# Kernel tuning notes

Hardware: AMD Instinct MI355X
Metric: run time of the kernel (lower is better)

The kernel has to match this reference:

```python
import jax, jax.numpy as jnp
import numpy as np

HEADS = 8
DIM_HEAD = 64
NH = 16
NW = 16
SCALE = DIM_HEAD ** -0.5


def _avg2x2(a):
    # 2x2 average pool, stride 1, over axes 1,2 of [B,H,W,C] (== unfold+mean in torch)
    return (a[:, :-1, :-1] + a[:, 1:, :-1] + a[:, :-1, 1:] + a[:, 1:, 1:]) * 0.25


def _split_heads(t):
    B, n, _ = t.shape
    return t.reshape(B, n, HEADS, DIM_HEAD).transpose(0, 2, 1, 3)  # b h n d


def setup_inputs() -> dict:
    key = jax.random.key(0)
    ks = jax.random.split(key, 5)
    B, n, dim = 64, 482, 512
    inner = HEADS * DIM_HEAD
    return {
        "x": jax.random.normal(ks[0], (B, n, dim), jnp.float32),
        "mask": jax.random.normal(ks[1], (B, n, dim), jnp.float32),
        "W_qkv": jax.random.normal(ks[2], (3 * inner, dim), jnp.float32) * 0.02,
        "W_out": jax.random.normal(ks[3], (dim, inner), jnp.float32) * 0.02,
        "b_out": jax.random.normal(ks[4], (dim,), jnp.float32) * 0.02,
    }


def reference(x, mask, W_qkv, W_out, b_out):
    sg = jax.lax.stop_gradient
    B, n, dim = x.shape
    inner = HEADS * DIM_HEAD
    nHW = NH * NW            # 256
    nb = (NH - 1) * (NW - 1)  # 225

    # qkv projection
    qkv = x @ W_qkv.T                              # [B,n,3*inner]
    q, k, v = (
        _split_heads(t) for t in jnp.split(qkv, 3, axis=-1)
    )

    # mask path (no grad)
    mask_ = sg(mask)
    updated = (jnp.mean(mask_[:, 1:], axis=-1, keepdims=True) > 0.0).astype(x.dtype)
    updated = jnp.concatenate([jnp.ones_like(updated[:, :1]), updated], axis=1)  # [B,n,1]
    qkv_m = mask_ @ jnp.abs(sg(W_qkv)).T
    q_m, k_m, v_m = (_split_heads(t) for t in jnp.split(qkv_m, 3, axis=-1))
    q_m = q_m / (1e-6 + jnp.max(q_m, axis=2, keepdims=True))
    k_m = k_m / (1e-6 + jnp.max(k_m, axis=2, keepdims=True))
    v_m = v_m / (1e-6 + jnp.max(v_m, axis=2, keepdims=True))
    q_m, k_m, v_m = sg(q_m), sg(k_m), sg(v_m)

    # mask-modulated attention
    dots = jnp.einsum('bhnd,bhmd->bhnm', q * q_m, k * k_m) * SCALE
    attn = jax.nn.softmax(dots, axis=-1)
    out = jnp.einsum('bhnm,bhmd->bhnd', attn, v_m * v)
    out = out.transpose(0, 2, 1, 3).reshape(B, n, inner) * updated

    m = jnp.einsum('bhnm,bhmd->bhnd', sg(attn), v_m)
    m = sg(m.transpose(0, 2, 1, 3).reshape(B, n, inner) * updated)

    # overlap blending (is_overlap=True)
    inv_tail = 1.0 - updated[:, -nb:]
    inv_grid = 1.0 - updated[:, 1:nHW + 1]

    out_bridge = _avg2x2(out[:, 1:nHW + 1].reshape(B, NH, NW, inner)).reshape(B, nb, inner) * inv_tail
    out_origin = jnp.pad(out[:, -nb:].reshape(B, NH - 1, NW - 1, inner),
                         ((0, 0), (1, 1), (1, 1), (0, 0)))
    out_origin = _avg2x2(out_origin).reshape(B, nHW, inner) * inv_grid

    m_bridge = _avg2x2(m[:, 1:nHW + 1].reshape(B, NH, NW, inner)).reshape(B, nb, inner) * inv_tail
    m_origin = jnp.pad(m[:, -nb:].reshape(B, NH - 1, NW - 1, inner),
                       ((0, 0), (1, 1), (1, 1), (0, 0)))
    m_origin = _avg2x2(m_origin).reshape(B, nHW, inner) * inv_grid

    out = out.at[:, 1:nHW + 1].add(out_origin).at[:, -nb:].add(out_bridge)
    m = sg(m.at[:, 1:nHW + 1].add(m_origin).at[:, -nb:].add(m_bridge))

    # nearest-neighbor interpolation of mask means (no grad)
    mm = jnp.mean(m[:, 1:], axis=-1, keepdims=True)          # [B,n-1,1]
    a = mm[:, :nHW].reshape(B, 1, NH, NW)
    inter = jnp.repeat(jnp.repeat(a, 16, axis=2), 16, axis=3)  # [B,1,256,256]
    b = mm[:, -nb:].reshape(B, 1, NH - 1, NW - 1)
    inter_shift = jnp.repeat(jnp.repeat(b, 16, axis=2), 16, axis=3)  # [B,1,240,240]
    inter = inter.at[:, :, 8:-8, 8:-8].set((inter[:, :, 8:-8, 8:-8] + inter_shift) * 0.5)
    inter = sg(inter)

    m = sg(m @ jnp.abs(sg(W_out)).T)

    out_final = out @ W_out.T + b_out
    return out_final, m, inter
```

## Files before the change

### kernel.cpp

```cpp
#include <hip/hip_runtime.h>

#define B_      64
#define NSEQ    482
#define DIM     512
#define HEADS_  8
#define HD      64
#define QKV3    1536
#define NPAD    512
#define MROWS   (B_ * NSEQ)

typedef __bf16 v8bf __attribute__((ext_vector_type(8)));
typedef float  v4f  __attribute__((ext_vector_type(4)));

typedef __attribute__((address_space(1))) const unsigned short gu16;
typedef __attribute__((address_space(3))) unsigned short lu16;

__device__ __forceinline__ unsigned short f2bf(float f) {
    unsigned u = __float_as_uint(f);
    u += 0x7fffu + ((u >> 16) & 1u);
    return (unsigned short)(u >> 16);
}
__device__ __forceinline__ float bf2f(unsigned short h) {
    return __uint_as_float(((unsigned)h) << 16);
}

__global__ void k_cvt(const float* __restrict__ s, unsigned short* __restrict__ d, int n4) {
    int i = blockIdx.x * 256 + threadIdx.x;
    if (i < n4) {
        float4 v = ((const float4*)s)[i];
        ushort4 o;
        o.x = f2bf(v.x); o.y = f2bf(v.y); o.z = f2bf(v.z); o.w = f2bf(v.w);
        ((ushort4*)d)[i] = o;
    }
}

__global__ void k_cvtabs(const float* __restrict__ s, unsigned short* __restrict__ d,
                         unsigned short* __restrict__ da, int n4) {
    int i = blockIdx.x * 256 + threadIdx.x;
    if (i < n4) {
        float4 v = ((const float4*)s)[i];
        ushort4 o, oa;
        o.x = f2bf(v.x); o.y = f2bf(v.y); o.z = f2bf(v.z); o.w = f2bf(v.w);
        oa.x = f2bf(fabsf(v.x)); oa.y = f2bf(fabsf(v.y));
        oa.z = f2bf(fabsf(v.z)); oa.w = f2bf(fabsf(v.w));
        ((ushort4*)d)[i] = o;
        ((ushort4*)da)[i] = oa;
    }
}

__global__ __launch_bounds__(256) void k_cvtmask(const float* __restrict__ mask,
                                                 unsigned short* __restrict__ mb,
                                                 float* __restrict__ upd) {
    int row = blockIdx.x * 4 + (threadIdx.x >> 6);
    int lane = threadIdx.x & 63;
    const float4* p = (const float4*)(mask + (size_t)row * DIM);
    ushort4* d = (ushort4*)(mb + (size_t)row * DIM);
    float s = 0.f;
    #pragma unroll
    for (int j = 0; j < 2; j++) {
        float4 v = p[j * 64 + lane];
        ushort4 o;
        o.x = f2bf(v.x); o.y = f2bf(v.y); o.z = f2bf(v.z); o.w = f2bf(v.w);
        d[j * 64 + lane] = o;
        s += v.x + v.y + v.z + v.w;
    }
    #pragma unroll
    for (int off = 32; off; off >>= 1) s += __shfl_xor(s, off);
    if (lane == 0) {
        int i = row % NSEQ;
        upd[row] = (i == 0) ? 1.f : ((s > 0.f) ? 1.f : 0.f);
    }
}

__global__ __launch_bounds__(256, 2) void k_gemm(const unsigned short* __restrict__ A,
                                                 const unsigned short* __restrict__ Bw,
                                                 unsigned short* __restrict__ Cb,
                                                 float* __restrict__ Cf,
                                                 const float* __restrict__ bias,
                                                 int N, int K) {
    __shared__ __align__(16) unsigned short As[128 * 32];
    __shared__ __align__(16) unsigned short Bs[128 * 32];
    int tid = threadIdx.x;
    int lane = tid & 63, w = tid >> 6;
    int wm = w & 1, wn = w >> 1;
    int quad = lane >> 4, m16 = lane & 15;
    int m0 = blockIdx.y * 128, n0 = blockIdx.x * 128;

    int srow = w * 16 + (lane >> 2);
    int scol = (lane & 3) * 8;
    const unsigned short* gA0 = &A[(size_t)(m0 + srow) * K + scol];
    const unsigned short* gA1 = &A[(size_t)(m0 + 64 + srow) * K + scol];
    const unsigned short* gB0 = &Bw[(size_t)(n0 + srow) * K + scol];
    const unsigned short* gB1 = &Bw[(size_t)(n0 + 64 + srow) * K + scol];
    lu16* lA0 = (lu16*)&As[w * 512];
    lu16* lA1 = (lu16*)&As[2048 + w * 512];
    lu16* lB0 = (lu16*)&Bs[w * 512];
    lu16* lB1 = (lu16*)&Bs[2048 + w * 512];

    v4f acc[4][4];
    #pragma unroll
    for (int i = 0; i < 4; i++)
        #pragma unroll
        for (int j = 0; j < 4; j++) acc[i][j] = (v4f){0.f, 0.f, 0.f, 0.f};

    for (int k0 = 0; k0 < K; k0 += 32) {
        __builtin_amdgcn_global_load_lds((gu16*)(gA0 + k0), lA0, 16, 0, 0);
        __builtin_amdgcn_global_load_lds((gu16*)(gA1 + k0), lA1, 16, 0, 0);
        __builtin_amdgcn_global_load_lds((gu16*)(gB0 + k0), lB0, 16, 0, 0);
        __builtin_amdgcn_global_load_lds((gu16*)(gB1 + k0), lB1, 16, 0, 0);
        __syncthreads();
        v8bf af[4], bf[4];
        #pragma unroll
        for (int i = 0; i < 4; i++)
            af[i] = *(const v8bf*)&As[(wm * 64 + i * 16 + m16) * 32 + quad * 8];
        #pragma unroll
        for (int j = 0; j < 4; j++)
            bf[j] = *(const v8bf*)&Bs[(wn * 64 + j * 16 + m16) * 32 + quad * 8];
        #pragma unroll
        for (int i = 0; i < 4; i++)
            #pragma unroll
            for (int j = 0; j < 4; j++)
                acc[i][j] = __builtin_amdgcn_mfma_f32_16x16x32_bf16(af[i], bf[j], acc[i][j], 0, 0, 0);
        __syncthreads();
    }

    #pragma unroll
    for (int j = 0; j < 4; j++) {
        int col = n0 + wn * 64 + j * 16 + m16;
        float bi = bias ? bias[col] : 0.f;
        #pragma unroll
        for (int i = 0; i < 4; i++) {
            int rowb = m0 + wm * 64 + i * 16 + quad * 4;
            #pragma unroll
            for (int r = 0; r < 4; r++) {
                float v = acc[i][j][r] + bi;
                size_t off = (size_t)(rowb + r) * N + col;
                if (Cf) Cf[off] = v;
                else    Cb[off] = f2bf(v);
            }
        }
    }
}

__global__ void k_colmax(const unsigned short* __restrict__ qm, float* __restrict__ invsc) {
    int b = blockIdx.x;
    int c = blockIdx.y * 256 + threadIdx.x;
    const unsigned short* p = qm + (size_t)b * NSEQ * QKV3 + c;
    float mx = -1e30f;
    for (int i = 0; i < NSEQ; i++) mx = fmaxf(mx, bf2f(p[(size_t)i * QKV3]));
    invsc[b * QKV3 + c] = 1.f / (1e-6f + mx);
}

__global__ __launch_bounds__(256) void k_build(const unsigned short* __restrict__ qkv,
                                               const unsigned short* __restrict__ qm,
                                               const float* __restrict__ invsc,
                                               unsigned short* __restrict__ QQ,
                                               unsigned short* __restrict__ KK,
                                               unsigned short* __restrict__ VVt,
                                               unsigned short* __restrict__ VMt) {
    __shared__ unsigned short tv[64][72];
    __shared__ unsigned short tm[64][72];
    int tid = threadIdx.x;
    int dd = tid & 63, il = tid >> 6;
    int it = blockIdx.x, h = blockIdx.y, b = blockIdx.z;
    int i0 = it * 64;
    size_t bh = (size_t)(b * HEADS_ + h);
    int c = h * HD + dd;
    float invq = invsc[b * QKV3 + c] * 0.125f;
    float invk = invsc[b * QKV3 + 512 + c];
    float invv = invsc[b * QKV3 + 1024 + c];
    #pragma unroll 4
    for (int p = 0; p < 16; p++) {
        int li = p * 4 + il;
        int i = i0 + li;
        unsigned short oq = 0, ok = 0, ov = 0, om = 0;
        if (i < NSEQ) {
            size_t base = ((size_t)(b * NSEQ + i)) * QKV3 + c;
            float q  = bf2f(qkv[base]),        qv = bf2f(qm[base]);
            float kk = bf2f(qkv[base + 512]),  kv = bf2f(qm[base + 512]);
            float vv = bf2f(qkv[base + 1024]), vm = bf2f(qm[base + 1024]);
            oq = f2bf(q * qv * invq);
            ok = f2bf(kk * kv * invk);
            float vmn = vm * invv;
            ov = f2bf(vv * vmn);
            om = f2bf(vmn);
        }
        QQ[(bh * NPAD + i) * HD + dd] = oq;
        KK[(bh * NPAD + i) * HD + dd] = ok;
        tv[li][dd] = ov;
        tm[li][dd] = om;
    }
    __syncthreads();
    #pragma unroll 4
    for (int p = 0; p < 16; p++) {
        int dr = p * 4 + il;
        VVt[(bh * HD + dr) * NPAD + i0 + dd] = tv[dd][dr];
        VMt[(bh * HD + dr) * NPAD + i0 + dd] = tm[dd][dr];
    }
}

__global__ __launch_bounds__(256, 3) void k_attn(const unsigned short* __restrict__ QQ,
                                                 const unsigned short* __restrict__ KK,
                                                 const unsigned short* __restrict__ VVt,
                                                 const unsigned short* __restrict__ VMt,
                                                 const float* __restrict__ upd,
                                                 float* __restrict__ OUT1,
                                                 float* __restrict__ M1) {
    __shared__ __align__(16) unsigned short Ks[2][32 * 72];
    __shared__ __align__(16) unsigned short Vs[2][64 * 40];
    __shared__ __align__(16) unsigned short Ms[2][64 * 40];
    __shared__ __align__(16) unsigned short Ps[4][32 * 40];

    int tid = threadIdx.x;
    int w = tid >> 6, lane = tid & 63;
    int quad = lane >> 4, m16 = lane & 15;
    int b = blockIdx.z, h = blockIdx.y;
    int q0 = blockIdx.x * 128 + w * 32;
    size_t bh = (size_t)(b * HEADS_ + h);

    v8bf aq[2][2];
    #pragma unroll
    for (int s = 0; s < 2; s++) {
        const unsigned short* qb = &QQ[(bh * NPAD + q0 + s * 16 + m16) * HD];
        aq[s][0] = *(const v8bf*)&qb[quad * 8];
        aq[s][1] = *(const v8bf*)&qb[32 + quad * 8];
    }

    v4f vacc[2][4], macc[2][4];
    #pragma unroll
    for (int s = 0; s < 2; s++)
        #pragma unroll
        for (int dt = 0; dt < 4; dt++) {
            vacc[s][dt] = (v4f){0.f, 0.f, 0.f, 0.f};
            macc[s][dt] = (v4f){0.f, 0.f, 0.f, 0.f};
        }
    float lrun[2][4];
    #pragma unroll
    for (int s = 0; s < 2; s++)
        #pragma unroll
        for (int r = 0; r < 4; r++) lrun[s][r] = 0.f;

    const unsigned short* gK = &KK[bh * NPAD * HD + tid * 8];
    const unsigned short* gV = &VVt[(bh * HD + (tid >> 2)) * NPAD + (tid & 3) * 8];
    const unsigned short* gM = &VMt[(bh * HD + (tid >> 2)) * NPAD + (tid & 3) * 8];
    int oK = (tid >> 3) * 72 + (tid & 7) * 8;
    int oV = (tid >> 2) * 40 + (tid & 3) * 8;
    unsigned short* Pw = &Ps[w][0];

    int4 rk = *(const int4*)gK;
    int4 rv = *(const int4*)gV;
    int4 rm = *(const int4*)gM;

    for (int ic = 0; ic < 16; ++ic) {
        int buf = ic & 1;
        *(int4*)&Ks[buf][oK] = rk;
        *(int4*)&Vs[buf][oV] = rv;
        *(int4*)&Ms[buf][oV] = rm;
        if (ic < 15) {
            rk = *(const int4*)(gK + (ic + 1) * 32 * HD);
            rv = *(const int4*)(gV + (ic + 1) * 32);
            rm = *(const int4*)(gM + (ic + 1) * 32);
        }
        __syncthreads();

        v8bf kf[2][2];
        #pragma unroll
        for (int t = 0; t < 2; t++) {
            kf[t][0] = *(const v8bf*)&Ks[buf][(t * 16 + m16) * 72 + quad * 8];
            kf[t][1] = *(const v8bf*)&Ks[buf][(t * 16 + m16) * 72 + 32 + quad * 8];
        }
        v4f S[2][2];
        #pragma unroll
        for (int s = 0; s < 2; s++)
            #pragma unroll
            for (int t = 0; t < 2; t++) {
                v4f a = (v4f){0.f, 0.f, 0.f, 0.f};
                a = __builtin_amdgcn_mfma_f32_16x16x32_bf16(aq[s][0], kf[t][0], a, 0, 0, 0);
                a = __builtin_amdgcn_mfma_f32_16x16x32_bf16(aq[s][1], kf[t][1], a, 0, 0, 0);
                S[s][t] = a;
            }

        int i0 = ic * 32;
        if (i0 + 32 > NSEQ) {
            bool x0 = (i0 + m16) >= NSEQ;
            bool x1 = (i0 + 16 + m16) >= NSEQ;
            #pragma unroll
            for (int s = 0; s < 2; s++)
                #pragma unroll
                for (int r = 0; r < 4; r++) {
                    if (x0) S[s][0][r] = -1e30f;
                    if (x1) S[s][1][r] = -1e30f;
                }
        }

        #pragma unroll
        for (int s = 0; s < 2; s++)
            #pragma unroll
            for (int r = 0; r < 4; r++) {
                float e0 = __expf(S[s][0][r]);
                float e1 = __expf(S[s][1][r]);
                lrun[s][r] += e0 + e1;
                Pw[(s * 16 + quad * 4 + r) * 40 + m16] = f2bf(e0);
                Pw[(s * 16 + quad * 4 + r) * 40 + 16 + m16] = f2bf(e1);
            }

        v8bf ap[2];
        ap[0] = *(const v8bf*)&Pw[m16 * 40 + quad * 8];
        ap[1] = *(const v8bf*)&Pw[(16 + m16) * 40 + quad * 8];

        #pragma unroll
        for (int dt = 0; dt < 4; dt++) {
            v8bf bv = *(const v8bf*)&Vs[buf][(dt * 16 + m16) * 40 + quad * 8];
            v8bf bm = *(const v8bf*)&Ms[buf][(dt * 16 + m16) * 40 + quad * 8];
            #pragma unroll
            for (int s = 0; s < 2; s++) {
                vacc[s][dt] = __builtin_amdgcn_mfma_f32_16x16x32_bf16(ap[s], bv, vacc[s][dt], 0, 0, 0);
                macc[s][dt] = __builtin_amdgcn_mfma_f32_16x16x32_bf16(ap[s], bm, macc[s][dt], 0, 0, 0);
            }
        }
    }

    #pragma unroll
    for (int s = 0; s < 2; s++)
        #pragma unroll
        for (int r = 0; r < 4; r++) {
            float sum = lrun[s][r];
            sum += __shfl_xor(sum, 1);
            sum += __shfl_xor(sum, 2);
            sum += __shfl_xor(sum, 4);
            sum += __shfl_xor(sum, 8);
            float iv = 1.f / sum;
            int iq = q0 + s * 16 + quad * 4 + r;
            if (iq < NSEQ) {
                float u = upd[b * NSEQ + iq] * iv;
                size_t off = ((size_t)(b * NSEQ + iq)) * DIM + h * HD + m16;
                #pragma unroll
                for (int dt = 0; dt < 4; dt++) {
                    OUT1[off + dt * 16] = vacc[s][dt][r] * u;
                    M1[off + dt * 16]   = macc[s][dt][r] * u;
                }
            }
        }
}

__global__ __launch_bounds__(256) void k_blend(const float* __restrict__ O1,
                                               const float* __restrict__ Mm,
                                               const float* __restrict__ upd,
                                               unsigned short* __restrict__ O2,
                                               unsigned short* __restrict__ M2,
                                               float* __restrict__ mm) {
    int blk = blockIdx.x;
    int b = blk / NSEQ, i = blk - b * NSEQ;
    int tid = threadIdx.x;
    size_t rb = (size_t)blk * DIM;
    int ns = 0;
    size_t src[4];
    float wgt = 0.f;
    if (i >= 1) {
        wgt = 0.25f * (1.f - upd[blk]);
        if (wgt != 0.f) {
            if (i <= 256) {
                int g = i - 1, gy = g >> 4, gx = g & 15;
                #pragma unroll
                for (int dy = 0; dy < 2; dy++)
                    #pragma unroll
                    for (int dx = 0; dx < 2; dx++) {
                        int sy = gy - 1 + dy, sx = gx - 1 + dx;
                        if (sy >= 0 && sy < 15 && sx >= 0 && sx < 15)
                            src[ns++] = ((size_t)(b * NSEQ + 257 + sy * 15 + sx)) * DIM;
                    }
            } else {
                int t = i - 257, ty = t / 15, tx = t - ty * 15;
                #pragma unroll
                for (int dy = 0; dy < 2; dy++)
                    #pragma unroll
                    for (int dx = 0; dx < 2; dx++)
                        src[ns++] = ((size_t)(b * NSEQ + 1 + (ty + dy) * 16 + (tx + dx))) * DIM;
            }
        }
    }
    float msum = 0.f;
    for (int c = tid; c < DIM; c += 256) {
        float o = O1[rb + c], m = Mm[rb + c];
        float ao = 0.f, am = 0.f;
        for (int s = 0; s < ns; s++) { ao += O1[src[s] + c]; am += Mm[src[s] + c]; }
        o += wgt * ao;
        m += wgt * am;
        O2[rb + c] = f2bf(o);
        M2[rb + c] = f2bf(m);
        msum += m;
    }
    #pragma unroll
    for (int off = 32; off; off >>= 1) msum += __shfl_xor(msum, off);
    __shared__ float red[4];
    if ((tid & 63) == 0) red[tid >> 6] = msum;
    __syncthreads();
    if (tid == 0 && i >= 1)
        mm[b * 481 + i - 1] = (red[0] + red[1] + red[2] + red[3]) * (1.f / 512.f);
}

__global__ void k_inter(const float* __restrict__ mm, float* __restrict__ dst) {
    int idx = blockIdx.x * 256 + threadIdx.x;
    int b = idx >> 16, rem = idx & 65535;
    int y = rem >> 8, x = rem & 255;
    const float* mb = mm + b * 481;
    float v = mb[((y >> 4) << 4) + (x >> 4)];
    if (y >= 8 && y < 248 && x >= 8 && x < 248)
        v = 0.5f * (v + mb[256 + ((y - 8) >> 4) * 15 + ((x - 8) >> 4)]);
    dst[idx] = v;
}

extern "C" void kernel_launch(void* const* d_in, const int* in_sizes, int n_in,
                              void* d_out, int out_size, void* d_ws, size_t ws_size,
                              hipStream_t stream) {
    const float* x    = (const float*)d_in[0];
    const float* mask = (const float*)d_in[1];
    const float* Wqkv = (const float*)d_in[2];
    const float* Wout = (const float*)d_in[3];
    const float* bout = (const float*)d_in[4];
    float* out = (float*)d_out;

    char* ws = (char*)d_ws;
    size_t o = 0;
    auto alloc = [&](size_t bytes) -> char* {
        char* r = ws + o;
        o += (bytes + 255) & ~(size_t)255;
        return r;
    };
    unsigned short* xb    = (unsigned short*)alloc((size_t)MROWS * DIM * 2);
    unsigned short* maskb = (unsigned short*)alloc((size_t)MROWS * DIM * 2);
    unsigned short* Wb    = (unsigned short*)alloc((size_t)QKV3 * DIM * 2);
    unsigned short* Wab   = (unsigned short*)alloc((size_t)QKV3 * DIM * 2);
    unsigned short* Wob   = (unsigned short*)alloc((size_t)DIM * DIM * 2);
    unsigned short* Woab  = (unsigned short*)alloc((size_t)DIM * DIM * 2);
    unsigned short* qkvb  = (unsigned short*)alloc((size_t)MROWS * QKV3 * 2);
    unsigned short* qkvmb = (unsigned short*)alloc((size_t)MROWS * QKV3 * 2);
    float* upd  = (float*)alloc((size_t)MROWS * 4);
    float* invs = (float*)alloc((size_t)B_ * QKV3 * 4);
    float* mm   = (float*)alloc((size_t)B_ * 481 * 4);
    unsigned short* QQ  = (unsigned short*)alloc((size_t)B_ * HEADS_ * NPAD * HD * 2);
    unsigned short* KK  = (unsigned short*)alloc((size_t)B_ * HEADS_ * NPAD * HD * 2);
    unsigned short* VVt = (unsigned short*)alloc((size_t)B_ * HEADS_ * NPAD * HD * 2);
    unsigned short* VMt = (unsigned short*)alloc((size_t)B_ * HEADS_ * NPAD * HD * 2);
    float* OUT1 = (float*)qkvb;
    float* M1p  = (float*)qkvmb;
    unsigned short* O2 = xb;
    unsigned short* M2 = maskb;

    k_cvt<<<(MROWS * DIM / 4) / 256, 256, 0, stream>>>(x, xb, MROWS * DIM / 4);
    k_cvtmask<<<MROWS / 4, 256, 0, stream>>>(mask, maskb, upd);
    k_cvtabs<<<(QKV3 * DIM / 4) / 256, 256, 0, stream>>>(Wqkv, Wb, Wab, QKV3 * DIM / 4);
    k_cvtabs<<<(DIM * DIM / 4) / 256, 256, 0, stream>>>(Wout, Wob, Woab, DIM * DIM / 4);

    dim3 g1(QKV3 / 128, MROWS / 128);
    k_gemm<<<g1, 256, 0, stream>>>(xb, Wb, qkvb, nullptr, nullptr, QKV3, DIM);
    k_gemm<<<g1, 256, 0, stream>>>(maskb, Wab, qkvmb, nullptr, nullptr, QKV3, DIM);

    k_colmax<<<dim3(B_, QKV3 / 256), 256, 0, stream>>>(qkvmb, invs);
    k_build<<<dim3(8, HEADS_, B_), 256, 0, stream>>>(qkvb, qkvmb, invs, QQ, KK, VVt, VMt);

    k_attn<<<dim3(4, HEADS_, B_), 256, 0, stream>>>(QQ, KK, VVt, VMt, upd, OUT1, M1p);

    k_blend<<<MROWS, 256, 0, stream>>>(OUT1, M1p, upd, O2, M2, mm);
    k_inter<<<(B_ * 65536) / 256, 256, 0, stream>>>(mm, out + (size_t)2 * MROWS * DIM);

    dim3 g2(DIM / 128, MROWS / 128);
    k_gemm<<<g2, 256, 0, stream>>>(O2, Wob, nullptr, out, bout, DIM, DIM);
    k_gemm<<<g2, 256, 0, stream>>>(M2, Woab, nullptr, out + (size_t)MROWS * DIM, nullptr, DIM, DIM);
}
```

Before: 786.8 us.

## Fuse paired GEMMs sharing a weight tile, add XCD-aware block remapping

The x and mask projections, and the two output projections, now run as one dual-accumulator GEMM. It loads the bf16 weight tile once and derives its absolute value in registers by clearing the sign bit, so the separate |W| conversions and buffers go away. The bf16 epilogue now stages results through a swizzled LDS buffer to write 16-byte coalesced rows. Both the GEMM and the attention kernel remap block IDs so neighbouring tiles land on the same XCD for better L2 locality. In exchange, accumulator registers and LDS per block double, which may reduce occupancy.

After: 760.5 us. -3.3%, faster.

```diff
diff --git a/kernel.cpp b/kernel.cpp
--- a/kernel.cpp
+++ b/kernel.cpp
@@ -11,6 +11,7 @@
 
 typedef __bf16 v8bf __attribute__((ext_vector_type(8)));
 typedef float  v4f  __attribute__((ext_vector_type(4)));
+typedef unsigned int v4u __attribute__((ext_vector_type(4)));
 
 typedef __attribute__((address_space(1))) const unsigned short gu16;
 typedef __attribute__((address_space(3))) unsigned short lu16;
@@ -22,6 +23,14 @@
 }
 __device__ __forceinline__ float bf2f(unsigned short h) {
     return __uint_as_float(((unsigned)h) << 16);
+}
+__device__ __forceinline__ v8bf vabs8(v8bf x) {
+    v4u u;
+    __builtin_memcpy(&u, &x, 16);
+    u &= (v4u){0x7fff7fffu, 0x7fff7fffu, 0x7fff7fffu, 0x7fff7fffu};
+    v8bf r;
+    __builtin_memcpy(&r, &u, 16);
+    return r;
 }
 
 __global__ void k_cvt(const float* __restrict__ s, unsigned short* __restrict__ d, int n4) {
@@ -31,20 +40,6 @@
         ushort4 o;
         o.x = f2bf(v.x); o.y = f2bf(v.y); o.z = f2bf(v.z); o.w = f2bf(v.w);
         ((ushort4*)d)[i] = o;
-    }
-}
-
-__global__ void k_cvtabs(const float* __restrict__ s, unsigned short* __restrict__ d,
-                         unsigned short* __restrict__ da, int n4) {
-    int i = blockIdx.x * 256 + threadIdx.x;
-    if (i < n4) {
-        float4 v = ((const float4*)s)[i];
-        ushort4 o, oa;
-        o.x = f2bf(v.x); o.y = f2bf(v.y); o.z = f2bf(v.z); o.w = f2bf(v.w);
-        oa.x = f2bf(fabsf(v.x)); oa.y = f2bf(fabsf(v.y));
-        oa.z = f2bf(fabsf(v.z)); oa.w = f2bf(fabsf(v.w));
-        ((ushort4*)d)[i] = o;
-        ((ushort4*)da)[i] = oa;
     }
 }
 
@@ -72,72 +67,135 @@
     }
 }
 
-__global__ __launch_bounds__(256, 2) void k_gemm(const unsigned short* __restrict__ A,
-                                                 const unsigned short* __restrict__ Bw,
-                                                 unsigned short* __restrict__ Cb,
-                                                 float* __restrict__ Cf,
-                                                 const float* __restrict__ bias,
-                                                 int N, int K) {
-    __shared__ __align__(16) unsigned short As[128 * 32];
+__global__ __launch_bounds__(256, 2) void k_gemm2(const unsigned short* __restrict__ A1,
+                                                  const unsigned short* __restrict__ A2,
+                                                  const unsigned short* __restrict__ Bw,
+                                                  unsigned short* __restrict__ C1b,
+                                                  unsigned short* __restrict__ C2b,
+                                                  float* __restrict__ C1f,
+                                                  float* __restrict__ C2f,
+                                                  const float* __restrict__ bias,
+                                                  int N, int K) {
+    __shared__ __align__(16) unsigned short As1[128 * 32];
+    __shared__ __align__(16) unsigned short As2[128 * 32];
     __shared__ __align__(16) unsigned short Bs[128 * 32];
     int tid = threadIdx.x;
     int lane = tid & 63, w = tid >> 6;
     int wm = w & 1, wn = w >> 1;
     int quad = lane >> 4, m16 = lane & 15;
-    int m0 = blockIdx.y * 128, n0 = blockIdx.x * 128;
+
+    int nbx = gridDim.x, nwg = nbx * gridDim.y;
+    int id = blockIdx.y * nbx + blockIdx.x;
+    int q = nwg >> 3, r = nwg & 7;
+    int xcd = id & 7, sub = id >> 3;
+    int nid = (xcd < r ? xcd * (q + 1) : r * (q + 1) + (xcd - r) * q) + sub;
+    int m0 = (nid / nbx) * 128, n0 = (nid % nbx) * 128;
 
     int srow = w * 16 + (lane >> 2);
     int scol = (lane & 3) * 8;
-    const unsigned short* gA0 = &A[(size_t)(m0 + srow) * K + scol];
-    const unsigned short* gA1 = &A[(size_t)(m0 + 64 + srow) * K + scol];
-    const unsigned short* gB0 = &Bw[(size_t)(n0 + srow) * K + scol];
-    const unsigned short* gB1 = &Bw[(size_t)(n0 + 64 + srow) * K + scol];
-    lu16* lA0 = (lu16*)&As[w * 512];
-    lu16* lA1 = (lu16*)&As[2048 + w * 512];
-    lu16* lB0 = (lu16*)&Bs[w * 512];
-    lu16* lB1 = (lu16*)&Bs[2048 + w * 512];
-
-    v4f acc[4][4];
+    const unsigned short* gA10 = &A1[(size_t)(m0 + srow) * K + scol];
+    const unsigned short* gA11 = &A1[(size_t)(m0 + 64 + srow) * K + scol];
+    const unsigned short* gA20 = &A2[(size_t)(m0 + srow) * K + scol];
+    const unsigned short* gA21 = &A2[(size_t)(m0 + 64 + srow) * K + scol];
+    const unsigned short* gB0  = &Bw[(size_t)(n0 + srow) * K + scol];
+    const unsigned short* gB1  = &Bw[(size_t)(n0 + 64 + srow) * K + scol];
+    lu16* lA10 = (lu16*)&As1[w * 512];
+    lu16* lA11 = (lu16*)&As1[2048 + w * 512];
+    lu16* lA20 = (lu16*)&As2[w * 512];
+    lu16* lA21 = (lu16*)&As2[2048 + w * 512];
+    lu16* lB0  = (lu16*)&Bs[w * 512];
+    lu16* lB1  = (lu16*)&Bs[2048 + w * 512];
+
+    v4f acc1[4][4], acc2[4][4];
     #pragma unroll
     for (int i = 0; i < 4; i++)
         #pragma unroll
-        for (int j = 0; j < 4; j++) acc[i][j] = (v4f){0.f, 0.f, 0.f, 0.f};
+        for (int j = 0; j < 4; j++) {
+            acc1[i][j] = (v4f){0.f, 0.f, 0.f, 0.f};
+            acc2[i][j] = (v4f){0.f, 0.f, 0.f, 0.f};
+        }
 
     for (int k0 = 0; k0 < K; k0 += 32) {
-        __builtin_amdgcn_global_load_lds((gu16*)(gA0 + k0), lA0, 16, 0, 0);
-        __builtin_amdgcn_global_load_lds((gu16*)(gA1 + k0), lA1, 16, 0, 0);
+        __builtin_amdgcn_global_load_lds((gu16*)(gA10 + k0), lA10, 16, 0, 0);
+        __builtin_amdgcn_global_load_lds((gu16*)(gA11 + k0), lA11, 16, 0, 0);
+        __builtin_amdgcn_global_load_lds((gu16*)(gA20 + k0), lA20, 16, 0, 0);
+        __builtin_amdgcn_global_load_lds((gu16*)(gA21 + k0), lA21, 16, 0, 0);
         __builtin_amdgcn_global_load_lds((gu16*)(gB0 + k0), lB0, 16, 0, 0);
         __builtin_amdgcn_global_load_lds((gu16*)(gB1 + k0), lB1, 16, 0, 0);
         __syncthreads();
-        v8bf af[4], bf[4];
-        #pragma unroll
-        for (int i = 0; i < 4; i++)
-            af[i] = *(const v8bf*)&As[(wm * 64 + i * 16 + m16) * 32 + quad * 8];
-        #pragma unroll
-        for (int j = 0; j < 4; j++)
-            bf[j] = *(const v8bf*)&Bs[(wn * 64 + j * 16 + m16) * 32 + quad * 8];
-        #pragma unroll
-        for (int i = 0; i < 4; i++)
+        v8bf a1[4], a2[4];
+        #pragma unroll
+        for (int i = 0; i < 4; i++) {
+            a1[i] = *(const v8bf*)&As1[(wm * 64 + i * 16 + m16) * 32 + quad * 8];
+            a2[i] = *(const v8bf*)&As2[(wm * 64 + i * 16 + m16) * 32 + quad * 8];
+        }
+        #pragma unroll
+        for (int j = 0; j < 4; j++) {
+            v8bf bb = *(const v8bf*)&Bs[(wn * 64 + j * 16 + m16) * 32 + quad * 8];
+            v8bf ba = vabs8(bb);
+            #pragma unroll
+            for (int i = 0; i < 4; i++) {
+                acc1[i][j] = __builtin_amdgcn_mfma_f32_16x16x32_bf16(a1[i], bb, acc1[i][j], 0, 0, 0);
+                acc2[i][j] = __builtin_amdgcn_mfma_f32_16x16x32_bf16(a2[i], ba, acc2[i][j], 0, 0, 0);
+            }
+        }
+        __syncthreads();
+    }
+
+    if (C1f) {
+        #pragma unroll
+        for (int j = 0; j < 4; j++) {
+            int col = n0 + wn * 64 + j * 16 + m16;
+            float bi = bias ? bias[col] : 0.f;
+            #pragma unroll
+            for (int i = 0; i < 4; i++) {
+                int rowb = m0 + wm * 64 + i * 16 + quad * 4;
+                #pragma unroll
+                for (int r = 0; r < 4; r++) {
+                    size_t off = (size_t)(rowb + r) * N + col;
+                    C1f[off] = acc1[i][j][r] + bi;
+                    C2f[off] = acc2[i][j][r];
+                }
+            }
+        }
+    } else {
+        unsigned short* wbuf = &As1[w * 1024];
+        int rr = lane >> 2;
+        int c0 = ((lane & 3) * 2) ^ ((rr >> 1) & 7);
+        size_t colb = n0 + wn * 64 + (lane & 3) * 16;
+        #pragma unroll
+        for (int i = 0; i < 4; i++) {
             #pragma unroll
             for (int j = 0; j < 4; j++)
-                acc[i][j] = __builtin_amdgcn_mfma_f32_16x16x32_bf16(af[i], bf[j], acc[i][j], 0, 0, 0);
-        __syncthreads();
-    }
-
-    #pragma unroll
-    for (int j = 0; j < 4; j++) {
-        int col = n0 + wn * 64 + j * 16 + m16;
-        float bi = bias ? bias[col] : 0.f;
+                #pragma unroll
+                for (int r = 0; r < 4; r++) {
+                    int row = quad * 4 + r;
+                    int e = j * 16 + m16;
+                    int es = ((((e >> 3) ^ ((row >> 1) & 7)) << 3) | (e & 7));
+                    wbuf[row * 64 + es] = f2bf(acc1[i][j][r]);
+                }
+            int4 p0 = *(const int4*)&wbuf[rr * 64 + c0 * 8];
+            int4 p1 = *(const int4*)&wbuf[rr * 64 + (c0 ^ 1) * 8];
+            size_t off0 = (size_t)(m0 + wm * 64 + i * 16 + rr) * N + colb;
+            *(int4*)&C1b[off0] = p0;
+            *(int4*)&C1b[off0 + 8] = p1;
+        }
         #pragma unroll
         for (int i = 0; i < 4; i++) {
-            int rowb = m0 + wm * 64 + i * 16 + quad * 4;
-            #pragma unroll
-            for (int r = 0; r < 4; r++) {
-                float v = acc[i][j][r] + bi;
-                size_t off = (size_t)(rowb + r) * N + col;
-                if (Cf) Cf[off] = v;
-                else    Cb[off] = f2bf(v);
-            }
+            #pragma unroll
+            for (int j = 0; j < 4; j++)
+                #pragma unroll
+                for (int r = 0; r < 4; r++) {
+                    int row = quad * 4 + r;
+                    int e = j * 16 + m16;
+                    int es = ((((e >> 3) ^ ((row >> 1) & 7)) << 3) | (e & 7));
+                    wbuf[row * 64 + es] = f2bf(acc2[i][j][r]);
+                }
+            int4 p0 = *(const int4*)&wbuf[rr * 64 + c0 * 8];
+            int4 p1 = *(const int4*)&wbuf[rr * 64 + (c0 ^ 1) * 8];
+            size_t off0 = (size_t)(m0 + wm * 64 + i * 16 + rr) * N + colb;
+            *(int4*)&C2b[off0] = p0;
+            *(int4*)&C2b[off0 + 8] = p1;
         }
     }
 }
@@ -214,8 +272,10 @@
     int tid = threadIdx.x;
     int w = tid >> 6, lane = tid & 63;
     int quad = lane >> 4, m16 = lane & 15;
-    int b = blockIdx.z, h = blockIdx.y;
-    int q0 = blockIdx.x * 128 + w * 32;
+    int id = (blockIdx.z * 8 + blockIdx.y) * 4 + blockIdx.x;
+    int nid = (id & 7) * 256 + (id >> 3);
+    int b = nid >> 5, h = (nid >> 2) & 7;
+    int q0 = (nid & 3) * 128 + w * 32;
     size_t bh = (size_t)(b * HEADS_ + h);
 
     v8bf aq[2][2];
@@ -430,9 +490,7 @@
     unsigned short* xb    = (unsigned short*)alloc((size_t)MROWS * DIM * 2);
     unsigned short* maskb = (unsigned short*)alloc((size_t)MROWS * DIM * 2);
     unsigned short* Wb    = (unsigned short*)alloc((size_t)QKV3 * DIM * 2);
-    unsigned short* Wab   = (unsigned short*)alloc((size_t)QKV3 * DIM * 2);
     unsigned short* Wob   = (unsigned short*)alloc((size_t)DIM * DIM * 2);
-    unsigned short* Woab  = (unsigned short*)alloc((size_t)DIM * DIM * 2);
     unsigned short* qkvb  = (unsigned short*)alloc((size_t)MROWS * QKV3 * 2);
     unsigned short* qkvmb = (unsigned short*)alloc((size_t)MROWS * QKV3 * 2);
     float* upd  = (float*)alloc((size_t)MROWS * 4);
@@ -449,12 +507,12 @@
 
     k_cvt<<<(MROWS * DIM / 4) / 256, 256, 0, stream>>>(x, xb, MROWS * DIM / 4);
     k_cvtmask<<<MROWS / 4, 256, 0, stream>>>(mask, maskb, upd);
-    k_cvtabs<<<(QKV3 * DIM / 4) / 256, 256, 0, stream>>>(Wqkv, Wb, Wab, QKV3 * DIM / 4);
-    k_cvtabs<<<(DIM * DIM / 4) / 256, 256, 0, stream>>>(Wout, Wob, Woab, DIM * DIM / 4);
+    k_cvt<<<(QKV3 * DIM / 4) / 256, 256, 0, stream>>>(Wqkv, Wb, QKV3 * DIM / 4);
+    k_cvt<<<(DIM * DIM / 4) / 256, 256, 0, stream>>>(Wout, Wob, DIM * DIM / 4);
 
     dim3 g1(QKV3 / 128, MROWS / 128);
-    k_gemm<<<g1, 256, 0, stream>>>(xb, Wb, qkvb, nullptr, nullptr, QKV3, DIM);
-    k_gemm<<<g1, 256, 0, stream>>>(maskb, Wab, qkvmb, nullptr, nullptr, QKV3, DIM);
+    k_gemm2<<<g1, 256, 0, stream>>>(xb, maskb, Wb, qkvb, qkvmb,
+                                    nullptr, nullptr, nullptr, QKV3, DIM);
 
     k_colmax<<<dim3(B_, QKV3 / 256), 256, 0, stream>>>(qkvmb, invs);
     k_build<<<dim3(8, HEADS_, B_), 256, 0, stream>>>(qkvb, qkvmb, invs, QQ, KK, VVt, VMt);
@@ -465,6 +523,6 @@
     k_inter<<<(B_ * 65536) / 256, 256, 0, stream>>>(mm, out + (size_t)2 * MROWS * DIM);
 
     dim3 g2(DIM / 128, MROWS / 128);
-    k_gemm<<<g2, 256, 0, stream>>>(O2, Wob, nullptr, out, bout, DIM, DIM);
-    k_gemm<<<g2, 256, 0, stream>>>(M2, Woab, nullptr, out + (size_t)MROWS * DIM, nullptr, DIM, DIM);
-}
+    k_gemm2<<<g2, 256, 0, stream>>>(O2, M2, Wob, nullptr, nullptr,
+                                    out, out + (size_t)MROWS * DIM, bout, DIM, DIM);
+}
```
